# Kernel optimization log

Measured on AMD Instinct MI355X. Metric: run time of the kernel, lower is better.

## Reference

```python
import jax, jax.numpy as jnp
import numpy as np

NUM_HEADS = 12
SIZE_PER_HEAD = 64


def setup_inputs() -> dict:
    key = jax.random.key(0)
    ks = jax.random.split(key, 4)
    B, S, D = 4, 2048, NUM_HEADS * SIZE_PER_HEAD
    std = 0.02
    return {
        "x": jax.random.normal(ks[0], (B, S, D), dtype=jnp.float32),
        "Wq": jax.random.normal(ks[1], (D, D), dtype=jnp.float32) * std,
        "bq": jnp.zeros((D,), dtype=jnp.float32),
        "Wk": jax.random.normal(ks[2], (D, D), dtype=jnp.float32) * std,
        "bk": jnp.zeros((D,), dtype=jnp.float32),
        "Wv": jax.random.normal(ks[3], (D, D), dtype=jnp.float32) * std,
        "bv": jnp.zeros((D,), dtype=jnp.float32),
        "mask": jnp.ones((B, S), dtype=jnp.int32),
    }


def reference(x, Wq, bq, Wk, bk, Wv, bv, mask):
    B, S, Dm = x.shape
    H, Dh = NUM_HEADS, SIZE_PER_HEAD
    # QKV projections (no activation, per defaults)
    q = (x @ Wq + bq).reshape(B, S, H, Dh)
    k = (x @ Wk + bk).reshape(B, S, H, Dh)
    v = (x @ Wv + bv).reshape(B, S, H, Dh)
    # scaled dot-product scores [B, H, F, T]
    scores = jnp.einsum("bfhd,bthd->bhft", q, k) / jnp.sqrt(
        jnp.asarray(Dh, dtype=x.dtype)
    )
    # additive mask: (1 - mask) * -10000, broadcast over heads and F
    adder = (1.0 - mask.astype(x.dtype))[:, None, None, :] * -10000.0
    probs = jax.nn.softmax(scores + adder, axis=-1)
    # dropout is identity at inference (training=None)
    ctx = jnp.einsum("bhft,bthd->bfhd", probs, v)
    return ctx.reshape(B, S, H * Dh)
```

## Files before the change

### kernel.cpp

```cpp
#include <hip/hip_runtime.h>
#include <cstdint>
#include <cstddef>

#define B_  4
#define S_  2048
#define H_  12
#define DH  64
#define DM  768

typedef unsigned short u16;
typedef __bf16 bf16x8 __attribute__((ext_vector_type(8)));
typedef float f32x4 __attribute__((ext_vector_type(4)));

__device__ __forceinline__ u16 f2bf(float f) {
  unsigned u = __float_as_uint(f);
  u += 0x7FFFu + ((u >> 16) & 1u);
  return (u16)(u >> 16);
}

__device__ __forceinline__ void gl16(const u16* g, u16* l) {
  __builtin_amdgcn_global_load_lds((const __attribute__((address_space(1))) void*)g,
                                   (__attribute__((address_space(3))) void*)l,
                                   16, 0, 0);
}

__global__ __launch_bounds__(256) void k_cvt_x(const float* __restrict__ x, u16* __restrict__ xb,
                                               const int* __restrict__ mask, int* __restrict__ mflags) {
  int i = blockIdx.x * 256 + threadIdx.x;
  const float4 v = ((const float4*)x)[i];
  ushort4 o;
  o.x = f2bf(v.x); o.y = f2bf(v.y); o.z = f2bf(v.z); o.w = f2bf(v.w);
  ((ushort4*)xb)[i] = o;
  if (blockIdx.x < 64) {
    __shared__ int f;
    if (threadIdx.x == 0) f = 0;
    __syncthreads();
    if (threadIdx.x < 128 && mask[blockIdx.x * 128 + threadIdx.x] != 1) f = 1;
    __syncthreads();
    if (threadIdx.x == 0) mflags[blockIdx.x] = f;
  }
}

__global__ __launch_bounds__(256) void k_wtrans(const float* __restrict__ Wq, const float* __restrict__ Wk,
                                                const float* __restrict__ Wv, u16* __restrict__ Wt) {
  const float* W = blockIdx.z == 0 ? Wq : (blockIdx.z == 1 ? Wk : Wv);
  u16* o = Wt + (size_t)blockIdx.z * DM * DM;
  __shared__ float t[32][33];
  const int x = threadIdx.x, y = threadIdx.y;
  const int n0 = blockIdx.x * 32, k0 = blockIdx.y * 32;
#pragma unroll
  for (int i = 0; i < 4; i++)
    t[y + i*8][x] = W[(size_t)(k0 + y + i*8)*DM + n0 + x];
  __syncthreads();
#pragma unroll
  for (int i = 0; i < 4; i++)
    o[(size_t)(n0 + y + i*8)*DM + k0 + x] = f2bf(t[x][y + i*8]);
}

__global__ __launch_bounds__(256, 4) void k_qkv(const u16* __restrict__ Xb, const u16* __restrict__ Wt,
                                                const float* __restrict__ bq, const float* __restrict__ bk,
                                                const float* __restrict__ bv, u16* __restrict__ QKV,
                                                u16* __restrict__ Vt) {
  const int mat = blockIdx.z;
  const float* bias = mat == 0 ? bq : (mat == 1 ? bk : bv);
  const int n0 = blockIdx.x * 128, m0 = blockIdx.y * 128;
  __shared__ __align__(16) u16 Al[2*128*32];
  __shared__ __align__(16) u16 Bl[2*128*32];
  const int tid = threadIdx.x, w = tid >> 6, l = tid & 63, l15 = l & 15, quad = l >> 4;
  const int wm = w & 1, wn = w >> 1;
  f32x4 acc[4][4];
#pragma unroll
  for (int i = 0; i < 4; i++)
#pragma unroll
    for (int j = 0; j < 4; j++) acc[i][j] = f32x4{0.f, 0.f, 0.f, 0.f};

  int loff[2], ldst[2];
#pragma unroll
  for (int i = 0; i < 2; i++) {
    int c = tid + i*256;
    int r = c >> 2, s = c & 3, sl = s ^ ((r ^ (r >> 2)) & 3);
    loff[i] = r*DM + sl*8;
    ldst[i] = c*8;
  }
  const u16* ap = Xb + (size_t)m0 * DM;
  const u16* bp = Wt + (size_t)mat * DM * DM + (size_t)n0 * DM;

#define STAGE(kt) {                                     \
    int bb = ((kt) & 1) * 4096;                         \
    _Pragma("unroll")                                   \
    for (int i = 0; i < 2; i++) {                       \
      gl16(ap + (kt)*32 + loff[i], Al + bb + ldst[i]);  \
      gl16(bp + (kt)*32 + loff[i], Bl + bb + ldst[i]);  \
    }                                                   \
  }

  STAGE(0)
  for (int kt = 0; kt < DM/32; ++kt) {
    __syncthreads();
    if (kt + 1 < DM/32) STAGE(kt+1)
    const int bb = (kt & 1) * 4096;
    bf16x8 af[4], bfr[4];
#pragma unroll
    for (int mt = 0; mt < 4; mt++) {
      int row = wm*64 + mt*16 + l15;
      int ph = quad ^ ((row ^ (row >> 2)) & 3);
      af[mt] = *(const bf16x8*)(Al + bb + row*32 + ph*8);
    }
#pragma unroll
    for (int nt = 0; nt < 4; nt++) {
      int row = wn*64 + nt*16 + l15;
      int ph = quad ^ ((row ^ (row >> 2)) & 3);
      bfr[nt] = *(const bf16x8*)(Bl + bb + row*32 + ph*8);
    }
#pragma unroll
    for (int mt = 0; mt < 4; mt++)
#pragma unroll
      for (int nt = 0; nt < 4; nt++)
        acc[mt][nt] = __builtin_amdgcn_mfma_f32_16x16x32_bf16(af[mt], bfr[nt], acc[mt][nt], 0, 0, 0);
  }
#undef STAGE

  float b4[4];
#pragma unroll
  for (int nt = 0; nt < 4; nt++) b4[nt] = bias[n0 + wn*64 + nt*16 + l15];

  if (mat == 2) {
    const int b = m0 / S_;
    const int h = (n0 + wn*64) >> 6;
    const int tbase = (m0 % S_) + wm*64;
#pragma unroll
    for (int mt = 0; mt < 4; mt++)
#pragma unroll
      for (int nt = 0; nt < 4; nt++) {
        int d = nt*16 + l15;
        int t = tbase + mt*16 + quad*4;
        ushort4 o;
        o.x = f2bf(acc[mt][nt][0] + b4[nt]);
        o.y = f2bf(acc[mt][nt][1] + b4[nt]);
        o.z = f2bf(acc[mt][nt][2] + b4[nt]);
        o.w = f2bf(acc[mt][nt][3] + b4[nt]);
        *(ushort4*)(Vt + ((size_t)(b*H_ + h)*DH + d)*S_ + t) = o;
      }
  } else {
    const float osc = (mat == 0) ? (0.125f * 1.44269504f) : 1.0f;
    u16* outm = QKV + (size_t)mat * (size_t)(B_*S_) * DM;
#pragma unroll
    for (int mt = 0; mt < 4; mt++)
#pragma unroll
      for (int r = 0; r < 4; r++) {
        int gm = m0 + wm*64 + mt*16 + quad*4 + r;
        u16* orow = outm + (size_t)gm*DM + n0 + wn*64;
#pragma unroll
        for (int nt = 0; nt < 4; nt++)
          orow[nt*16 + l15] = f2bf((acc[mt][nt][r] + b4[nt]) * osc);
      }
  }
}

__global__ __launch_bounds__(128, 2) void k_attn(const u16* __restrict__ Qb, const u16* __restrict__ Kb,
                                                 const u16* __restrict__ Vt, const int* __restrict__ mask,
                                                 const int* __restrict__ mflags, float* __restrict__ out) {
  const int bh = blockIdx.x, b = bh / H_, h = bh % H_;
  const int q0 = blockIdx.y * 128;
  __shared__ __align__(16) u16 Kl[128*64];
  __shared__ __align__(16) u16 Vl[64*128];
  __shared__ __align__(16) u16 QP[2*64*72];
  __shared__ __align__(16) float maskl[128];
  const int tid = threadIdx.x, w = tid >> 6, l = tid & 63, l15 = l & 15, quad = l >> 4;

#pragma unroll
  for (int i = 0; i < 8; i++) {
    int c = tid + i*128;
    int r = c >> 3, s = c & 7, sl = s ^ (r & 7);
    gl16(Qb + (size_t)(b*S_ + q0 + r)*DM + h*DH + sl*8, QP + c*8);
  }
  __syncthreads();
  bf16x8 qf[4][2];
#pragma unroll
  for (int nt = 0; nt < 4; nt++)
#pragma unroll
    for (int ks = 0; ks < 2; ks++) {
      int r = w*64 + nt*16 + l15;
      int ph = (ks*4 + quad) ^ (r & 7);
      qf[nt][ks] = *(const bf16x8*)(QP + r*64 + ph*8);
    }
  __syncthreads();

  f32x4 O[4][4], Ol[4];
#pragma unroll
  for (int i = 0; i < 4; i++) {
    Ol[i] = f32x4{0.f, 0.f, 0.f, 0.f};
#pragma unroll
    for (int j = 0; j < 4; j++) O[i][j] = f32x4{0.f, 0.f, 0.f, 0.f};
  }
  const f32x4 ZV = {0.f, 0.f, 0.f, 0.f};
  bf16x8 vone;
#pragma unroll
  for (int j = 0; j < 8; j++) vone[j] = (l15 == 0) ? (__bf16)1.0f : (__bf16)0.0f;
  u16* Pw = QP + w*64*72;

  int koff[8], voff[8];
#pragma unroll
  for (int i = 0; i < 8; i++) {
    int c = tid + i*128;
    { int r = c >> 3, s = c & 7, sl = s ^ (r & 7);   koff[i] = r*DM + sl*8; }
    { int r = c >> 4, s = c & 15, sl = s ^ (r & 15); voff[i] = r*S_ + sl*8; }
  }
  const u16* kp = Kb + (size_t)(b*S_)*DM + h*DH;
  const u16* vp = Vt + (size_t)bh*DH*S_;

  for (int tt = 0; tt < S_/128; ++tt) {
    __syncthreads();
#pragma unroll
    for (int i = 0; i < 8; i++) {
      int c = tid + i*128;
      gl16(kp + koff[i], Kl + c*8);
      gl16(vp + voff[i], Vl + c*8);
    }
    kp += 128*DM; vp += 128;
    const int mflag = mflags[b*16 + tt];
    if (mflag)
      maskl[tid] = (1.0f - (float)mask[b*S_ + tt*128 + tid]) * (-10000.0f * 1.44269504f);
    __syncthreads();

#pragma unroll
    for (int h2 = 0; h2 < 2; ++h2) {
      f32x4 sc[4][4];
#pragma unroll
      for (int mt = 0; mt < 4; mt++) {
        int row = h2*64 + mt*16 + l15;
        bf16x8 k0f = *(const bf16x8*)(Kl + row*64 + ((quad    ) ^ (row & 7))*8);
        bf16x8 k1f = *(const bf16x8*)(Kl + row*64 + ((4 + quad) ^ (row & 7))*8);
#pragma unroll
        for (int nt = 0; nt < 4; nt++) {
          sc[mt][nt] = __builtin_amdgcn_mfma_f32_16x16x32_bf16(k0f, qf[nt][0], ZV, 0, 0, 0);
          sc[mt][nt] = __builtin_amdgcn_mfma_f32_16x16x32_bf16(k1f, qf[nt][1], sc[mt][nt], 0, 0, 0);
        }
      }
      if (mflag) {
#pragma unroll
        for (int mt = 0; mt < 4; mt++) {
          f32x4 mv = *(const f32x4*)&maskl[h2*64 + mt*16 + quad*4];
#pragma unroll
          for (int nt = 0; nt < 4; nt++)
#pragma unroll
            for (int r = 0; r < 4; r++) sc[mt][nt][r] += mv[r];
        }
      }
#pragma unroll
      for (int nt = 0; nt < 4; nt++)
#pragma unroll
        for (int mt = 0; mt < 4; mt++) {
          unsigned u[4];
#pragma unroll
          for (int r = 0; r < 4; r++) u[r] = __float_as_uint(__builtin_amdgcn_exp2f(sc[mt][nt][r]));
          uint2 pk;
          pk.x = __builtin_amdgcn_perm(u[1], u[0], 0x07060302u);
          pk.y = __builtin_amdgcn_perm(u[3], u[2], 0x07060302u);
          *(uint2*)(Pw + (nt*16 + l15)*72 + mt*16 + quad*4) = pk;
        }
      asm volatile("s_waitcnt lgkmcnt(0)" ::: "memory");
#pragma unroll
      for (int kk = 0; kk < 2; kk++) {
        int ksg = h2*2 + kk;
        bf16x8 pa[4], vb[4];
#pragma unroll
        for (int mo = 0; mo < 4; mo++)
          pa[mo] = *(const bf16x8*)(Pw + (mo*16 + l15)*72 + kk*32 + quad*8);
#pragma unroll
        for (int nd = 0; nd < 4; nd++) {
          int d = nd*16 + l15;
          int ph = (ksg*4 + quad) ^ (d & 15);
          vb[nd] = *(const bf16x8*)(Vl + d*128 + ph*8);
        }
#pragma unroll
        for (int mo = 0; mo < 4; mo++) {
#pragma unroll
          for (int nd = 0; nd < 4; nd++)
            O[mo][nd] = __builtin_amdgcn_mfma_f32_16x16x32_bf16(pa[mo], vb[nd], O[mo][nd], 0, 0, 0);
          Ol[mo] = __builtin_amdgcn_mfma_f32_16x16x32_bf16(pa[mo], vone, Ol[mo], 0, 0, 0);
        }
      }
    }
  }

#pragma unroll
  for (int mo = 0; mo < 4; mo++)
#pragma unroll
    for (int r = 0; r < 4; r++) {
      float lsum = __shfl(Ol[mo][r], l & 48);
      float inv = 1.0f / lsum;
      int q = q0 + w*64 + mo*16 + quad*4 + r;
      float* orow = out + (size_t)(b*S_ + q)*DM + h*DH;
#pragma unroll
      for (int nd = 0; nd < 4; nd++)
        orow[nd*16 + l15] = O[mo][nd][r] * inv;
    }
}

extern "C" void kernel_launch(void* const* d_in, const int* in_sizes, int n_in,
                              void* d_out, int out_size, void* d_ws, size_t ws_size,
                              hipStream_t stream) {
  const float* x  = (const float*)d_in[0];
  const float* Wq = (const float*)d_in[1];
  const float* bq = (const float*)d_in[2];
  const float* Wk = (const float*)d_in[3];
  const float* bk = (const float*)d_in[4];
  const float* Wv = (const float*)d_in[5];
  const float* bv = (const float*)d_in[6];
  const int* mask = (const int*)d_in[7];
  float* out = (float*)d_out;

  u16* Xb  = (u16*)d_ws;
  u16* Wt  = Xb  + (size_t)B_*S_*DM;
  u16* QKV = Wt  + (size_t)3*DM*DM;
  u16* Vt  = QKV + (size_t)3*B_*S_*DM;
  int* mflags = (int*)(Vt + (size_t)B_*S_*DM);

  k_cvt_x <<<dim3((B_*S_*DM)/1024), dim3(256), 0, stream>>>(x, Xb, mask, mflags);
  k_wtrans<<<dim3(24, 24, 3), dim3(32, 8), 0, stream>>>(Wq, Wk, Wv, Wt);
  k_qkv   <<<dim3(6, 64, 3), dim3(256), 0, stream>>>(Xb, Wt, bq, bk, bv, QKV, Vt);
  k_attn  <<<dim3(B_*H_, S_/128), dim3(128), 0, stream>>>(QKV, QKV + (size_t)B_*S_*DM, Vt, mask, mflags, out);
}
```

Before: 210.7 us.

## Merge prep kernels, widen QKV GEMM N-tile, use 256-query attention blocks

Merges the x conversion and weight transpose into a single prep launch, which removes one kernel launch. The QKV GEMM tile grows to 128x256 over a flattened 2304-wide output, with 8 N-subtiles per wave and occupancy lowered to 2. The attention kernel moves to 256 threads handling 256 queries per block, so each K/V tile is shared by four waves instead of two. The wider GEMM tile uses more registers and reduces occupancy, and the attention grid is halved, which may leave compute units underfilled.

After: 222.1 us. 1.05x slower.

```diff
diff --git a/kernel.cpp b/kernel.cpp
--- a/kernel.cpp
+++ b/kernel.cpp
@@ -24,123 +24,135 @@
                                    16, 0, 0);
 }
 
-__global__ __launch_bounds__(256) void k_cvt_x(const float* __restrict__ x, u16* __restrict__ xb,
-                                               const int* __restrict__ mask, int* __restrict__ mflags) {
-  int i = blockIdx.x * 256 + threadIdx.x;
-  const float4 v = ((const float4*)x)[i];
-  ushort4 o;
-  o.x = f2bf(v.x); o.y = f2bf(v.y); o.z = f2bf(v.z); o.w = f2bf(v.w);
-  ((ushort4*)xb)[i] = o;
-  if (blockIdx.x < 64) {
-    __shared__ int f;
-    if (threadIdx.x == 0) f = 0;
+__global__ __launch_bounds__(256) void k_prep(const float* __restrict__ x, u16* __restrict__ xb,
+                                              const int* __restrict__ mask, int* __restrict__ mflags,
+                                              const float* __restrict__ Wq, const float* __restrict__ Wk,
+                                              const float* __restrict__ Wv, u16* __restrict__ Wt) {
+  const int bid = blockIdx.x;
+  if (bid < 6144) {
+    int i = bid * 256 + threadIdx.x;
+    const float4 v = ((const float4*)x)[i];
+    ushort4 o;
+    o.x = f2bf(v.x); o.y = f2bf(v.y); o.z = f2bf(v.z); o.w = f2bf(v.w);
+    ((ushort4*)xb)[i] = o;
+    if (bid < 64) {
+      __shared__ int f;
+      if (threadIdx.x == 0) f = 0;
+      __syncthreads();
+      if (threadIdx.x < 128 && mask[bid * 128 + threadIdx.x] != 1) f = 1;
+      __syncthreads();
+      if (threadIdx.x == 0) mflags[bid] = f;
+    }
+  } else {
+    const int b2 = bid - 6144;
+    const int z = b2 / 576, rem = b2 % 576;
+    const int by = rem / 24, bx = rem % 24;
+    const float* W = z == 0 ? Wq : (z == 1 ? Wk : Wv);
+    u16* o = Wt + (size_t)z * DM * DM;
+    __shared__ float t[32][33];
+    const int xx = threadIdx.x & 31, yy = threadIdx.x >> 5;
+    const int n0 = bx * 32, k0 = by * 32;
+#pragma unroll
+    for (int i = 0; i < 4; i++)
+      t[yy + i*8][xx] = W[(size_t)(k0 + yy + i*8)*DM + n0 + xx];
     __syncthreads();
-    if (threadIdx.x < 128 && mask[blockIdx.x * 128 + threadIdx.x] != 1) f = 1;
-    __syncthreads();
-    if (threadIdx.x == 0) mflags[blockIdx.x] = f;
-  }
-}
-
-__global__ __launch_bounds__(256) void k_wtrans(const float* __restrict__ Wq, const float* __restrict__ Wk,
-                                                const float* __restrict__ Wv, u16* __restrict__ Wt) {
-  const float* W = blockIdx.z == 0 ? Wq : (blockIdx.z == 1 ? Wk : Wv);
-  u16* o = Wt + (size_t)blockIdx.z * DM * DM;
-  __shared__ float t[32][33];
-  const int x = threadIdx.x, y = threadIdx.y;
-  const int n0 = blockIdx.x * 32, k0 = blockIdx.y * 32;
-#pragma unroll
-  for (int i = 0; i < 4; i++)
-    t[y + i*8][x] = W[(size_t)(k0 + y + i*8)*DM + n0 + x];
-  __syncthreads();
-#pragma unroll
-  for (int i = 0; i < 4; i++)
-    o[(size_t)(n0 + y + i*8)*DM + k0 + x] = f2bf(t[x][y + i*8]);
-}
-
-__global__ __launch_bounds__(256, 4) void k_qkv(const u16* __restrict__ Xb, const u16* __restrict__ Wt,
+#pragma unroll
+    for (int i = 0; i < 4; i++)
+      o[(size_t)(n0 + yy + i*8)*DM + k0 + xx] = f2bf(t[xx][yy + i*8]);
+  }
+}
+
+__global__ __launch_bounds__(256, 2) void k_qkv(const u16* __restrict__ Xb, const u16* __restrict__ Wt,
                                                 const float* __restrict__ bq, const float* __restrict__ bk,
                                                 const float* __restrict__ bv, u16* __restrict__ QKV,
                                                 u16* __restrict__ Vt) {
-  const int mat = blockIdx.z;
+  const int n0 = blockIdx.x * 256, m0 = blockIdx.y * 128;
+  const int mat = blockIdx.x / 3;
+  const int n0r = n0 - mat * 768;
   const float* bias = mat == 0 ? bq : (mat == 1 ? bk : bv);
-  const int n0 = blockIdx.x * 128, m0 = blockIdx.y * 128;
   __shared__ __align__(16) u16 Al[2*128*32];
-  __shared__ __align__(16) u16 Bl[2*128*32];
+  __shared__ __align__(16) u16 Bl[2*256*32];
   const int tid = threadIdx.x, w = tid >> 6, l = tid & 63, l15 = l & 15, quad = l >> 4;
   const int wm = w & 1, wn = w >> 1;
-  f32x4 acc[4][4];
+  f32x4 acc[4][8];
 #pragma unroll
   for (int i = 0; i < 4; i++)
 #pragma unroll
-    for (int j = 0; j < 4; j++) acc[i][j] = f32x4{0.f, 0.f, 0.f, 0.f};
-
-  int loff[2], ldst[2];
+    for (int j = 0; j < 8; j++) acc[i][j] = f32x4{0.f, 0.f, 0.f, 0.f};
+
+  int aoff[2], boff[4];
 #pragma unroll
   for (int i = 0; i < 2; i++) {
     int c = tid + i*256;
     int r = c >> 2, s = c & 3, sl = s ^ ((r ^ (r >> 2)) & 3);
-    loff[i] = r*DM + sl*8;
-    ldst[i] = c*8;
+    aoff[i] = r*DM + sl*8;
+  }
+#pragma unroll
+  for (int i = 0; i < 4; i++) {
+    int c = tid + i*256;
+    int r = c >> 2, s = c & 3, sl = s ^ ((r ^ (r >> 2)) & 3);
+    boff[i] = r*DM + sl*8;
   }
   const u16* ap = Xb + (size_t)m0 * DM;
-  const u16* bp = Wt + (size_t)mat * DM * DM + (size_t)n0 * DM;
-
-#define STAGE(kt) {                                     \
-    int bb = ((kt) & 1) * 4096;                         \
-    _Pragma("unroll")                                   \
-    for (int i = 0; i < 2; i++) {                       \
-      gl16(ap + (kt)*32 + loff[i], Al + bb + ldst[i]);  \
-      gl16(bp + (kt)*32 + loff[i], Bl + bb + ldst[i]);  \
-    }                                                   \
+  const u16* bp = Wt + (size_t)n0 * DM;
+
+#define STAGE(kt) {                                             \
+    int ab = ((kt) & 1) * 4096, bb = ((kt) & 1) * 8192;         \
+    _Pragma("unroll")                                           \
+    for (int i = 0; i < 2; i++)                                 \
+      gl16(ap + (kt)*32 + aoff[i], Al + ab + (tid + i*256)*8);  \
+    _Pragma("unroll")                                           \
+    for (int i = 0; i < 4; i++)                                 \
+      gl16(bp + (kt)*32 + boff[i], Bl + bb + (tid + i*256)*8);  \
   }
 
   STAGE(0)
   for (int kt = 0; kt < DM/32; ++kt) {
     __syncthreads();
     if (kt + 1 < DM/32) STAGE(kt+1)
-    const int bb = (kt & 1) * 4096;
-    bf16x8 af[4], bfr[4];
+    const int ab = (kt & 1) * 4096, bb = (kt & 1) * 8192;
+    bf16x8 af[4], bfr[8];
 #pragma unroll
     for (int mt = 0; mt < 4; mt++) {
       int row = wm*64 + mt*16 + l15;
       int ph = quad ^ ((row ^ (row >> 2)) & 3);
-      af[mt] = *(const bf16x8*)(Al + bb + row*32 + ph*8);
-    }
-#pragma unroll
-    for (int nt = 0; nt < 4; nt++) {
-      int row = wn*64 + nt*16 + l15;
+      af[mt] = *(const bf16x8*)(Al + ab + row*32 + ph*8);
+    }
+#pragma unroll
+    for (int nt = 0; nt < 8; nt++) {
+      int row = wn*128 + nt*16 + l15;
       int ph = quad ^ ((row ^ (row >> 2)) & 3);
       bfr[nt] = *(const bf16x8*)(Bl + bb + row*32 + ph*8);
     }
 #pragma unroll
     for (int mt = 0; mt < 4; mt++)
 #pragma unroll
-      for (int nt = 0; nt < 4; nt++)
+      for (int nt = 0; nt < 8; nt++)
         acc[mt][nt] = __builtin_amdgcn_mfma_f32_16x16x32_bf16(af[mt], bfr[nt], acc[mt][nt], 0, 0, 0);
   }
 #undef STAGE
 
-  float b4[4];
-#pragma unroll
-  for (int nt = 0; nt < 4; nt++) b4[nt] = bias[n0 + wn*64 + nt*16 + l15];
+  float b8[8];
+#pragma unroll
+  for (int nt = 0; nt < 8; nt++) b8[nt] = bias[n0r + wn*128 + nt*16 + l15];
 
   if (mat == 2) {
-    const int b = m0 / S_;
-    const int h = (n0 + wn*64) >> 6;
-    const int tbase = (m0 % S_) + wm*64;
-#pragma unroll
-    for (int mt = 0; mt < 4; mt++)
-#pragma unroll
-      for (int nt = 0; nt < 4; nt++) {
-        int d = nt*16 + l15;
-        int t = tbase + mt*16 + quad*4;
+#pragma unroll
+    for (int mt = 0; mt < 4; mt++) {
+      int gm = m0 + wm*64 + mt*16 + quad*4;
+      int b = gm >> 11, t = gm & 2047;
+#pragma unroll
+      for (int nt = 0; nt < 8; nt++) {
+        int ng = n0r + wn*128 + nt*16;
+        int h = ng >> 6, d = (ng & 63) + l15;
         ushort4 o;
-        o.x = f2bf(acc[mt][nt][0] + b4[nt]);
-        o.y = f2bf(acc[mt][nt][1] + b4[nt]);
-        o.z = f2bf(acc[mt][nt][2] + b4[nt]);
-        o.w = f2bf(acc[mt][nt][3] + b4[nt]);
+        o.x = f2bf(acc[mt][nt][0] + b8[nt]);
+        o.y = f2bf(acc[mt][nt][1] + b8[nt]);
+        o.z = f2bf(acc[mt][nt][2] + b8[nt]);
+        o.w = f2bf(acc[mt][nt][3] + b8[nt]);
         *(ushort4*)(Vt + ((size_t)(b*H_ + h)*DH + d)*S_ + t) = o;
       }
+    }
   } else {
     const float osc = (mat == 0) ? (0.125f * 1.44269504f) : 1.0f;
     u16* outm = QKV + (size_t)mat * (size_t)(B_*S_) * DM;
@@ -149,28 +161,28 @@
 #pragma unroll
       for (int r = 0; r < 4; r++) {
         int gm = m0 + wm*64 + mt*16 + quad*4 + r;
-        u16* orow = outm + (size_t)gm*DM + n0 + wn*64;
-#pragma unroll
-        for (int nt = 0; nt < 4; nt++)
-          orow[nt*16 + l15] = f2bf((acc[mt][nt][r] + b4[nt]) * osc);
-      }
-  }
-}
-
-__global__ __launch_bounds__(128, 2) void k_attn(const u16* __restrict__ Qb, const u16* __restrict__ Kb,
+        u16* orow = outm + (size_t)gm*DM + n0r + wn*128;
+#pragma unroll
+        for (int nt = 0; nt < 8; nt++)
+          orow[nt*16 + l15] = f2bf((acc[mt][nt][r] + b8[nt]) * osc);
+      }
+  }
+}
+
+__global__ __launch_bounds__(256, 2) void k_attn(const u16* __restrict__ Qb, const u16* __restrict__ Kb,
                                                  const u16* __restrict__ Vt, const int* __restrict__ mask,
                                                  const int* __restrict__ mflags, float* __restrict__ out) {
   const int bh = blockIdx.x, b = bh / H_, h = bh % H_;
-  const int q0 = blockIdx.y * 128;
+  const int q0 = blockIdx.y * 256;
   __shared__ __align__(16) u16 Kl[128*64];
   __shared__ __align__(16) u16 Vl[64*128];
-  __shared__ __align__(16) u16 QP[2*64*72];
+  __shared__ __align__(16) u16 QP[4*64*72];
   __shared__ __align__(16) float maskl[128];
   const int tid = threadIdx.x, w = tid >> 6, l = tid & 63, l15 = l & 15, quad = l >> 4;
 
 #pragma unroll
   for (int i = 0; i < 8; i++) {
-    int c = tid + i*128;
+    int c = tid + i*256;
     int r = c >> 3, s = c & 7, sl = s ^ (r & 7);
     gl16(Qb + (size_t)(b*S_ + q0 + r)*DM + h*DH + sl*8, QP + c*8);
   }
@@ -199,10 +211,10 @@
   for (int j = 0; j < 8; j++) vone[j] = (l15 == 0) ? (__bf16)1.0f : (__bf16)0.0f;
   u16* Pw = QP + w*64*72;
 
-  int koff[8], voff[8];
-#pragma unroll
-  for (int i = 0; i < 8; i++) {
-    int c = tid + i*128;
+  int koff[4], voff[4];
+#pragma unroll
+  for (int i = 0; i < 4; i++) {
+    int c = tid + i*256;
     { int r = c >> 3, s = c & 7, sl = s ^ (r & 7);   koff[i] = r*DM + sl*8; }
     { int r = c >> 4, s = c & 15, sl = s ^ (r & 15); voff[i] = r*S_ + sl*8; }
   }
@@ -212,14 +224,14 @@
   for (int tt = 0; tt < S_/128; ++tt) {
     __syncthreads();
 #pragma unroll
-    for (int i = 0; i < 8; i++) {
-      int c = tid + i*128;
+    for (int i = 0; i < 4; i++) {
+      int c = tid + i*256;
       gl16(kp + koff[i], Kl + c*8);
       gl16(vp + voff[i], Vl + c*8);
     }
     kp += 128*DM; vp += 128;
     const int mflag = mflags[b*16 + tt];
-    if (mflag)
+    if (mflag && tid < 128)
       maskl[tid] = (1.0f - (float)mask[b*S_ + tt*128 + tid]) * (-10000.0f * 1.44269504f);
     __syncthreads();
 
@@ -317,8 +329,7 @@
   u16* Vt  = QKV + (size_t)3*B_*S_*DM;
   int* mflags = (int*)(Vt + (size_t)B_*S_*DM);
 
-  k_cvt_x <<<dim3((B_*S_*DM)/1024), dim3(256), 0, stream>>>(x, Xb, mask, mflags);
-  k_wtrans<<<dim3(24, 24, 3), dim3(32, 8), 0, stream>>>(Wq, Wk, Wv, Wt);
-  k_qkv   <<<dim3(6, 64, 3), dim3(256), 0, stream>>>(Xb, Wt, bq, bk, bv, QKV, Vt);
-  k_attn  <<<dim3(B_*H_, S_/128), dim3(128), 0, stream>>>(QKV, QKV + (size_t)B_*S_*DM, Vt, mask, mflags, out);
-}
+  k_prep<<<dim3(6144 + 1728), dim3(256), 0, stream>>>(x, Xb, mask, mflags, Wq, Wk, Wv, Wt);
+  k_qkv <<<dim3(9, 64), dim3(256), 0, stream>>>(Xb, Wt, bq, bk, bv, QKV, Vt);
+  k_attn<<<dim3(B_*H_, S_/256), dim3(256), 0, stream>>>(QKV, QKV + (size_t)B_*S_*DM, Vt, mask, mflags, out);
+}
```
